# Kernel tuning notes

Measured on AMD Instinct MI355X. Metric: run time of the kernel, lower is better.

The kernel has to match this reference:

```python
import jax, jax.numpy as jnp
import numpy as np

N = 100000      # nodes (single ntype)
R = 4           # edge types (relations)
E = 160000      # edges per relation
D_IN = 128
D_OUT = 128


def setup_inputs() -> dict:
    key = jax.random.key(0)
    k1, k2, k3, k4, k5 = jax.random.split(key, 5)
    gain = np.sqrt(2.0)  # calculate_gain('relu')
    bound = gain * np.sqrt(6.0 / (D_IN + D_OUT))  # xavier_uniform
    return {
        "x": jax.random.normal(k1, (N, D_IN), dtype=jnp.float32),
        "weight": jax.random.uniform(k2, (R, D_IN, D_OUT), dtype=jnp.float32,
                                     minval=-bound, maxval=bound),
        "loop_weight": jax.random.uniform(k3, (D_IN, D_OUT), dtype=jnp.float32,
                                          minval=-bound, maxval=bound),
        "h_bias": jnp.zeros((D_OUT,), dtype=jnp.float32),
        "src_idx": jax.random.randint(k4, (R, E), 0, N),
        "dst_idx": jax.random.randint(k5, (R, E), 0, N),
    }


def reference(x, weight, loop_weight, h_bias, src_idx, dst_idx):
    # Per-relation GraphConv(norm='right', weight external):
    #   h_r = segment_sum((x @ W_r)[src], dst) / clamp(in_degree, 1)
    # HeteroGraphConv default aggregation sums relations per dst node.
    n = x.shape[0]
    xw = jnp.einsum('nd,rdo->rno', x, weight)  # [R, N, D_OUT]
    h = jnp.zeros((n, weight.shape[2]), dtype=x.dtype)
    ones = jnp.ones((src_idx.shape[1],), dtype=x.dtype)
    for r in range(weight.shape[0]):  # small fixed relation count
        msg = xw[r][src_idx[r]]                                   # [E, D_OUT]
        agg = jax.ops.segment_sum(msg, dst_idx[r], num_segments=n)
        deg = jax.ops.segment_sum(ones, dst_idx[r], num_segments=n)
        h = h + agg / jnp.clip(deg, 1.0)[:, None]                 # norm='right'
    # self-loop + bias + activation (dropout=0 -> identity)
    h = h + x @ loop_weight + h_bias
    return jax.nn.relu(h)
```

## Files before the change

### kernel.cpp

```cpp
#include <hip/hip_runtime.h>

#define DD 128
#define KY 512
#define KT 640
#define RR 4
#define BKT 16
#define CAPS 15
#define NKS (KT / 32)

typedef short short8 __attribute__((ext_vector_type(8)));
typedef float f32x4 __attribute__((ext_vector_type(4)));

union U4S8 { uint4 u; short8 s; };

__device__ __forceinline__ unsigned short f2bf(float f) {
  unsigned u = __float_as_uint(f);
  u += 0x7fffu + ((u >> 16) & 1u);
  return (unsigned short)(u >> 16);
}

__global__ __launch_bounds__(256) void prep(const float* __restrict__ x,
                                            const float* __restrict__ weight,
                                            const float* __restrict__ loopw,
                                            const int* __restrict__ src,
                                            const int* __restrict__ dst,
                                            unsigned short* __restrict__ xb,
                                            unsigned short* __restrict__ wt,
                                            int* __restrict__ slot,
                                            int N, int E, int FB, int XB) {
  int b = blockIdx.x;
  int t = threadIdx.x;
  if (b < FB) {
    int i = b * 256 + t;
    if (i >= RR * E) return;
    int r = i / E;
    size_t base = ((size_t)dst[i] * RR + r) * BKT;
    int pos = atomicAdd(slot + base, 1);
    if (pos < CAPS) slot[base + 1 + pos] = src[i];
  } else if (b < FB + XB) {
    int i = (b - FB) * 256 + t;
    if (i >= (N + 1) * 16) return;
    int n = i >> 4;
    uint4 o = make_uint4(0, 0, 0, 0);
    if (n < N) {
      const float4* xp = (const float4*)x + (size_t)i * 2;
      float4 v0 = xp[0], v1 = xp[1];
      o.x = (unsigned)f2bf(v0.x) | ((unsigned)f2bf(v0.y) << 16);
      o.y = (unsigned)f2bf(v0.z) | ((unsigned)f2bf(v0.w) << 16);
      o.z = (unsigned)f2bf(v1.x) | ((unsigned)f2bf(v1.y) << 16);
      o.w = (unsigned)f2bf(v1.z) | ((unsigned)f2bf(v1.w) << 16);
    }
    ((uint4*)xb)[i] = o;
  } else {
    int i = (b - FB - XB) * 256 + t;
    if (i >= DD * KT) return;
    int j = i & 7, l = (i >> 3) & 63, c = (i >> 9) & 7, ks = i >> 12;
    int k = ks * 32 + (l >> 4) * 8 + j;
    int col = c * 16 + (l & 15);
    float v = (k < KY) ? weight[(size_t)((k >> 7) * DD + (k & (DD - 1))) * DD + col]
                       : loopw[(size_t)(k - KY) * DD + col];
    wt[i] = f2bf(v);
  }
}

__global__ __launch_bounds__(256) void gather_agg(const unsigned* __restrict__ xbu,
                                                  const int* __restrict__ slot,
                                                  unsigned* __restrict__ yu,
                                                  int NN ) {
  int gid = blockIdx.x * 256 + threadIdx.x;
  int n = gid >> 6, lane = gid & 63;
  if (n >= NN) return;
  int N = NN - 1;

  int sv = slot[(size_t)n * 64 + lane];

  int cn[RR], ct[RR];
#pragma unroll
  for (int r = 0; r < RR; r++) {
    ct[r] = __builtin_amdgcn_readlane(sv, r << 4);
    cn[r] = ct[r] > CAPS ? CAPS : ct[r];
  }

  float ax[RR], ay[RR];
#pragma unroll
  for (int r = 0; r < RR; r++) { ax[r] = 0.f; ay[r] = 0.f; }

#pragma unroll
  for (int r = 0; r < RR; r++) {
    for (int u = 0; u < cn[r]; u += 2) {
      int s0 = __builtin_amdgcn_readlane(sv, (r << 4) + 1 + u);
      int s1 = __builtin_amdgcn_readlane(sv, (r << 4) + 2 + u);
      s1 = (u + 1 < cn[r]) ? s1 : N;
      unsigned v0 = xbu[(size_t)s0 * 64 + lane];
      unsigned v1 = xbu[(size_t)s1 * 64 + lane];
      ax[r] += __uint_as_float(v0 << 16);
      ay[r] += __uint_as_float(v0 & 0xffff0000u);
      ax[r] += __uint_as_float(v1 << 16);
      ay[r] += __uint_as_float(v1 & 0xffff0000u);
    }
  }

#pragma unroll
  for (int r = 0; r < RR; r++) {
    float inv = 1.0f / (float)max(ct[r], 1);
    yu[(size_t)n * (KY / 2) + r * 64 + lane] =
        (unsigned)f2bf(ax[r] * inv) | ((unsigned)f2bf(ay[r] * inv) << 16);
  }
}

__global__ __launch_bounds__(512) void gemm_mfma(const unsigned short* __restrict__ y,
                                                 const unsigned short* __restrict__ xb,
                                                 const uint4* __restrict__ wtv,
                                                 const float* __restrict__ bias,
                                                 float* __restrict__ out, int N) {
  __shared__ __align__(16) unsigned short Bs[2][4096];
  int t = threadIdx.x;
  int w = t >> 6, lane = t & 63;
  int m = lane & 15, q = lane >> 4;
  int rb = blockIdx.x * 256;

  int grow0 = rb + w * 32 + m, grow1 = grow0 + 16;
  int r0c = grow0 > N ? N : grow0;
  int r1c = grow1 > N ? N : grow1;
  const unsigned short* ay0 = y  + (size_t)r0c * KY + q * 8;
  const unsigned short* ay1 = y  + (size_t)r1c * KY + q * 8;
  const unsigned short* ax0 = xb + (size_t)r0c * DD + q * 8;
  const unsigned short* ax1 = xb + (size_t)r1c * DD + q * 8;

  *(uint4*)(&Bs[0][t * 8]) = wtv[t];
  __syncthreads();

  f32x4 acc[2][8];
#pragma unroll
  for (int i = 0; i < 2; i++)
#pragma unroll
    for (int c = 0; c < 8; c++) acc[i][c] = (f32x4){0.f, 0.f, 0.f, 0.f};

#pragma unroll
  for (int ks = 0; ks < NKS; ++ks) {
    const int buf = ks & 1;
    uint4 bs;
    if (ks + 1 < NKS) bs = wtv[(size_t)(ks + 1) * 512 + t];

    U4S8 a0, a1;
    if (ks < 16) {
      a0.u = *(const uint4*)(ay0 + ks * 32);
      a1.u = *(const uint4*)(ay1 + ks * 32);
    } else {
      a0.u = *(const uint4*)(ax0 + (ks - 16) * 32);
      a1.u = *(const uint4*)(ax1 + (ks - 16) * 32);
    }

    short8 bb[8];
#pragma unroll
    for (int c = 0; c < 8; ++c)
      bb[c] = *(const short8*)(&Bs[buf][(c * 64 + lane) * 8]);

#pragma unroll
    for (int c = 0; c < 8; ++c) {
      acc[0][c] = __builtin_amdgcn_mfma_f32_16x16x32_bf16(a0.s, bb[c], acc[0][c], 0, 0, 0);
      acc[1][c] = __builtin_amdgcn_mfma_f32_16x16x32_bf16(a1.s, bb[c], acc[1][c], 0, 0, 0);
    }

    if (ks + 1 < NKS) {
      *(uint4*)(&Bs[buf ^ 1][t * 8]) = bs;
      __syncthreads();
    }
  }

  float bv[8];
#pragma unroll
  for (int c = 0; c < 8; ++c) bv[c] = bias[c * 16 + m];
#pragma unroll
  for (int i = 0; i < 2; ++i) {
    int rbase = rb + w * 32 + i * 16 + q * 4;
#pragma unroll
    for (int v = 0; v < 4; ++v) {
      int gr = rbase + v;
      if (gr < N) {
#pragma unroll
        for (int c = 0; c < 8; ++c)
          out[(size_t)gr * DD + c * 16 + m] = fmaxf(acc[i][c][v] + bv[c], 0.f);
      }
    }
  }
}

extern "C" void kernel_launch(void* const* d_in, const int* in_sizes, int n_in,
                              void* d_out, int out_size, void* d_ws, size_t ws_size,
                              hipStream_t stream) {
  const float* x      = (const float*)d_in[0];
  const float* weight = (const float*)d_in[1];
  const float* loop_w = (const float*)d_in[2];
  const float* h_bias = (const float*)d_in[3];
  const int*   src    = (const int*)d_in[4];
  const int*   dst    = (const int*)d_in[5];
  float* out = (float*)d_out;

  const int N = in_sizes[0] / DD;
  const int R = in_sizes[1] / (DD * DD);
  const int E = in_sizes[4] / R;
  const int RE = R * E;

  char* p = (char*)d_ws;
  auto alloc = [&](size_t bytes) {
    char* q = p;
    p += (bytes + 63) & ~size_t(63);
    return q;
  };
  int* slot = (int*)alloc((size_t)(N + 1) * RR * BKT * 4);
  unsigned short* wt = (unsigned short*)alloc((size_t)DD * KT * 2);
  unsigned short* xb = (unsigned short*)alloc((size_t)(N + 1) * DD * 2);
  unsigned short* y  = (unsigned short*)alloc((size_t)(N + 1) * KY * 2);

  hipMemsetAsync(slot, 0, (size_t)(N + 1) * RR * BKT * 4, stream);

  int FB = (RE + 255) / 256;
  int XB = ((N + 1) * 16 + 255) / 256;
  int WB = (DD * KT + 255) / 256;
  prep<<<FB + XB + WB, 256, 0, stream>>>(x, weight, loop_w, src, dst,
                                         xb, wt, slot, N, E, FB, XB);
  gather_agg<<<((size_t)(N + 1) * 64 + 255) / 256, 256, 0, stream>>>(
      (const unsigned*)xb, slot, (unsigned*)y, N + 1);
  gemm_mfma<<<(N + 255) / 256, 512, 0, stream>>>(y, xb, (const uint4*)wt,
                                                 h_bias, out, N);
}
```

Measured before the change: 226.7 us.

## Pair edges per thread, interleave relation gathers, shrink GEMM blocks to 256 threads

The edge-bucketing pass now handles two edges per thread with int2 loads. The gather kernel processes two relations per loop trip, issuing four independent row loads to raise memory-level parallelism, with padding to a dummy zero row when counts differ. The GEMM kernel now uses 256-thread blocks covering 128 rows, and each thread stages two B-tile vectors. This doubles the block count to improve occupancy and load balance, at the cost of more redundant weight staging per output row.

```diff
diff --git a/kernel.cpp b/kernel.cpp
--- a/kernel.cpp
+++ b/kernel.cpp
@@ -31,12 +31,17 @@
   int b = blockIdx.x;
   int t = threadIdx.x;
   if (b < FB) {
-    int i = b * 256 + t;
+    int i = (b * 256 + t) * 2;
     if (i >= RR * E) return;
-    int r = i / E;
-    size_t base = ((size_t)dst[i] * RR + r) * BKT;
-    int pos = atomicAdd(slot + base, 1);
-    if (pos < CAPS) slot[base + 1 + pos] = src[i];
+    int2 dp = *(const int2*)(dst + i);
+    int2 sp = *(const int2*)(src + i);
+    int r0 = i / E, r1 = (i + 1) / E;
+    size_t b0 = ((size_t)dp.x * RR + r0) * BKT;
+    size_t b1 = ((size_t)dp.y * RR + r1) * BKT;
+    int p0 = atomicAdd(slot + b0, 1);
+    int p1 = atomicAdd(slot + b1, 1);
+    if (p0 < CAPS) slot[b0 + 1 + p0] = sp.x;
+    if (p1 < CAPS) slot[b1 + 1 + p1] = sp.y;
   } else if (b < FB + XB) {
     int i = (b - FB) * 256 + t;
     if (i >= (N + 1) * 16) return;
@@ -86,17 +91,30 @@
   for (int r = 0; r < RR; r++) { ax[r] = 0.f; ay[r] = 0.f; }
 
 #pragma unroll
-  for (int r = 0; r < RR; r++) {
-    for (int u = 0; u < cn[r]; u += 2) {
-      int s0 = __builtin_amdgcn_readlane(sv, (r << 4) + 1 + u);
-      int s1 = __builtin_amdgcn_readlane(sv, (r << 4) + 2 + u);
-      s1 = (u + 1 < cn[r]) ? s1 : N;
+  for (int rp = 0; rp < RR; rp += 2) {
+    int mx = max(cn[rp], cn[rp + 1]);
+    for (int u = 0; u < mx; u += 2) {
+      int i0 = (rp << 4) + 1 + u;
+      int s0 = __builtin_amdgcn_readlane(sv, i0 & 63);
+      int s1 = __builtin_amdgcn_readlane(sv, (i0 + 1) & 63);
+      int s2 = __builtin_amdgcn_readlane(sv, (i0 + 16) & 63);
+      int s3 = __builtin_amdgcn_readlane(sv, (i0 + 17) & 63);
+      s0 = (u < cn[rp]) ? s0 : N;
+      s1 = (u + 1 < cn[rp]) ? s1 : N;
+      s2 = (u < cn[rp + 1]) ? s2 : N;
+      s3 = (u + 1 < cn[rp + 1]) ? s3 : N;
       unsigned v0 = xbu[(size_t)s0 * 64 + lane];
       unsigned v1 = xbu[(size_t)s1 * 64 + lane];
-      ax[r] += __uint_as_float(v0 << 16);
-      ay[r] += __uint_as_float(v0 & 0xffff0000u);
-      ax[r] += __uint_as_float(v1 << 16);
-      ay[r] += __uint_as_float(v1 & 0xffff0000u);
+      unsigned v2 = xbu[(size_t)s2 * 64 + lane];
+      unsigned v3 = xbu[(size_t)s3 * 64 + lane];
+      ax[rp] += __uint_as_float(v0 << 16);
+      ay[rp] += __uint_as_float(v0 & 0xffff0000u);
+      ax[rp] += __uint_as_float(v1 << 16);
+      ay[rp] += __uint_as_float(v1 & 0xffff0000u);
+      ax[rp + 1] += __uint_as_float(v2 << 16);
+      ay[rp + 1] += __uint_as_float(v2 & 0xffff0000u);
+      ax[rp + 1] += __uint_as_float(v3 << 16);
+      ay[rp + 1] += __uint_as_float(v3 & 0xffff0000u);
     }
   }
 
@@ -108,7 +126,7 @@
   }
 }
 
-__global__ __launch_bounds__(512) void gemm_mfma(const unsigned short* __restrict__ y,
+__global__ __launch_bounds__(256) void gemm_mfma(const unsigned short* __restrict__ y,
                                                  const unsigned short* __restrict__ xb,
                                                  const uint4* __restrict__ wtv,
                                                  const float* __restrict__ bias,
@@ -117,7 +135,7 @@
   int t = threadIdx.x;
   int w = t >> 6, lane = t & 63;
   int m = lane & 15, q = lane >> 4;
-  int rb = blockIdx.x * 256;
+  int rb = blockIdx.x * 128;
 
   int grow0 = rb + w * 32 + m, grow1 = grow0 + 16;
   int r0c = grow0 > N ? N : grow0;
@@ -128,6 +146,7 @@
   const unsigned short* ax1 = xb + (size_t)r1c * DD + q * 8;
 
   *(uint4*)(&Bs[0][t * 8]) = wtv[t];
+  *(uint4*)(&Bs[0][2048 + t * 8]) = wtv[256 + t];
   __syncthreads();
 
   f32x4 acc[2][8];
@@ -139,8 +158,11 @@
 #pragma unroll
   for (int ks = 0; ks < NKS; ++ks) {
     const int buf = ks & 1;
-    uint4 bs;
-    if (ks + 1 < NKS) bs = wtv[(size_t)(ks + 1) * 512 + t];
+    uint4 bs0, bs1;
+    if (ks + 1 < NKS) {
+      bs0 = wtv[(size_t)(ks + 1) * 512 + t];
+      bs1 = wtv[(size_t)(ks + 1) * 512 + 256 + t];
+    }
 
     U4S8 a0, a1;
     if (ks < 16) {
@@ -163,7 +185,8 @@
     }
 
     if (ks + 1 < NKS) {
-      *(uint4*)(&Bs[buf ^ 1][t * 8]) = bs;
+      *(uint4*)(&Bs[buf ^ 1][t * 8]) = bs0;
+      *(uint4*)(&Bs[buf ^ 1][2048 + t * 8]) = bs1;
       __syncthreads();
     }
   }
@@ -215,13 +238,13 @@
 
   hipMemsetAsync(slot, 0, (size_t)(N + 1) * RR * BKT * 4, stream);
 
-  int FB = (RE + 255) / 256;
+  int FB = (RE / 2 + 255) / 256;
   int XB = ((N + 1) * 16 + 255) / 256;
   int WB = (DD * KT + 255) / 256;
   prep<<<FB + XB + WB, 256, 0, stream>>>(x, weight, loop_w, src, dst,
                                          xb, wt, slot, N, E, FB, XB);
   gather_agg<<<((size_t)(N + 1) * 64 + 255) / 256, 256, 0, stream>>>(
       (const unsigned*)xb, slot, (unsigned*)y, N + 1);
-  gemm_mfma<<<(N + 255) / 256, 512, 0, stream>>>(y, xb, (const uint4*)wt,
+  gemm_mfma<<<(N + 127) / 128, 256, 0, stream>>>(y, xb, (const uint4*)wt,
                                                  h_bias, out, N);
 }
```

New measurement: 222.5 us. Within noise of the previous version (-1.9%).
